# Kernel optimization log

Measured on AMD Instinct MI355X. Metric: run time of the kernel, lower is better.

## Reference

```python
import jax, jax.numpy as jnp
import numpy as np

B0, C0, H0, W0 = 2, 64, 48, 48
BR, DI, NS, RK, K = 128, 128, 16, 4, 4
EPS = 1e-5


def _bn_relu(x, g, b):
    # eval-mode BatchNorm2d (running mean 0, var 1) followed by ReLU; x is NCHW
    return jax.nn.relu(x * (g / jnp.sqrt(1.0 + EPS))[None, :, None, None] + b[None, :, None, None])


def _c1(x, w):
    # 1x1 conv, w: (O, C, 1, 1)
    return jnp.einsum('bchw,oc->bohw', x, w[:, :, 0, 0])


def _avgpool(x, k, s, p):
    # torch AvgPool2d with count_include_pad=True -> divide by k*k
    y = jax.lax.reduce_window(x, 0.0, jax.lax.add, (1, 1, k, k), (1, 1, s, s), ((0, 0), (0, 0), (p, p), (p, p)))
    return y / float(k * k)


def _resize(x, h, w):
    # bilinear, align_corners=False (half-pixel), NCHW
    return jax.image.resize(x, (x.shape[0], x.shape[1], h, w), 'bilinear')


def _pappm(x, s0_g, s0_b, s0_w, s1_g, s1_b, s1_w, s2_g, s2_b, s2_w, s3_g, s3_b, s3_w, s4_g, s4_b, s4_w, comp_g, comp_b, comp_w, sc_g, sc_b, sc_w):
    h, w = x.shape[2], x.shape[3]
    x0 = _c1(_bn_relu(x, s0_g, s0_b), s0_w)
    y1 = _c1(_bn_relu(_avgpool(x, 3, 1, 1), s1_g, s1_b), s1_w) + x0  # stride-1 pool keeps size
    y2 = _resize(_c1(_bn_relu(_avgpool(x, 5, 2, 2), s2_g, s2_b), s2_w), h, w) + x0
    y3 = _resize(_c1(_bn_relu(_avgpool(x, 9, 4, 4), s3_g, s3_b), s3_w), h, w) + x0
    y4 = _c1(_bn_relu(x.mean((2, 3), keepdims=True), s4_g, s4_b), s4_w) + x0  # 1x1 -> broadcast
    cat = jnp.concatenate([x0, y1, y2, y3, y4], axis=1)  # (B, 5*BR, H, W)
    comp = jax.lax.conv_general_dilated(_bn_relu(cat, comp_g, comp_b), comp_w, (1, 1), ((1, 1), (1, 1)), dimension_numbers=('NCHW', 'OIHW', 'NCHW'))
    return comp + _c1(_bn_relu(x, sc_g, sc_b), sc_w)


def _ss2d(xin, in_proj_w, dw_w, dw_b, x_proj_w, dt_w, dt_b, A_logs, Ds, ln_g, ln_b, out_proj_w):
    # xin: (B, H, W, d_model)
    Bb, Hh, Ww, _ = xin.shape
    xz = xin @ in_proj_w.T                      # (B,H,W,2*DI)
    xc, z = jnp.split(xz, 2, axis=-1)
    xc = jnp.transpose(xc, (0, 3, 1, 2))        # (B,DI,H,W)
    xc = jax.lax.conv_general_dilated(xc, dw_w, (1, 1), ((1, 1), (1, 1)), dimension_numbers=('NCHW', 'OIHW', 'NCHW'), feature_group_count=DI)
    xc = jax.nn.silu(xc + dw_b[None, :, None, None])
    L = Hh * Ww
    x_hw = xc.reshape(Bb, DI, L)
    x_wh = jnp.transpose(xc, (0, 1, 3, 2)).reshape(Bb, DI, L)
    xs = jnp.stack([x_hw, x_wh, x_hw[:, :, ::-1], x_wh[:, :, ::-1]], axis=1)  # (B,K,DI,L)
    x_dbl = jnp.einsum('bkdl,kcd->bkcl', xs, x_proj_w)
    dts, Bm, Cm = jnp.split(x_dbl, [RK, RK + NS], axis=2)  # (B,K,RK,L),(B,K,NS,L),(B,K,NS,L)
    delta = jax.nn.softplus(jnp.einsum('bkrl,kdr->bkdl', dts, dt_w) + dt_b[None, :, :, None])  # (B,K,DI,L)
    A = -jnp.exp(A_logs).reshape(K, DI, NS)
    a = jnp.exp(delta[..., None] * A[None, :, :, None, :])                    # (B,K,DI,L,NS)
    bu = (delta * xs)[..., None] * jnp.transpose(Bm, (0, 1, 3, 2))[:, :, None]  # (B,K,DI,L,NS)

    def comb(e1, e2):
        a1, b1 = e1
        a2, b2 = e2
        return a2 * a1, a2 * b1 + b2

    _, hst = jax.lax.associative_scan(comb, (a, bu), axis=3)  # h_t = a_t*h_{t-1} + b_t
    y = jnp.einsum('bkdln,bknl->bkdl', hst, Cm) + xs * Ds.reshape(K, DI)[None, :, :, None]
    inv = y[:, 2:4][:, :, :, ::-1]
    y3 = jnp.transpose(y[:, 1].reshape(Bb, DI, Ww, Hh), (0, 1, 3, 2)).reshape(Bb, DI, L)
    y4 = jnp.transpose(inv[:, 1].reshape(Bb, DI, Ww, Hh), (0, 1, 3, 2)).reshape(Bb, DI, L)
    ys = jnp.transpose(y[:, 0] + inv[:, 0] + y3 + y4, (0, 2, 1)).reshape(Bb, Hh, Ww, DI)
    mu = ys.mean(-1, keepdims=True)
    var = jnp.mean((ys - mu) ** 2, -1, keepdims=True)
    yn = (ys - mu) / jnp.sqrt(var + EPS) * ln_g + ln_b
    return (yn * jax.nn.silu(z)) @ out_proj_w.T  # (B,H,W,d_model)


def setup_inputs():
    key = jax.random.key(0)
    ks = iter(jax.random.split(key, 32))
    nrm = lambda shp, s: jax.random.normal(next(ks), shp, jnp.float32) * s
    d = {}
    d['x'] = nrm((B0, C0, H0, W0), 1.0)
    for nm in ['s0', 's1', 's2', 's3', 's4']:
        d[nm + '_g'] = jnp.ones((C0,), jnp.float32)
        d[nm + '_b'] = jnp.zeros((C0,), jnp.float32)
        d[nm + '_w'] = nrm((BR, C0, 1, 1), (2.0 / C0) ** 0.5)
    d['comp_g'] = jnp.ones((5 * BR,), jnp.float32)
    d['comp_b'] = jnp.zeros((5 * BR,), jnp.float32)
    d['comp_w'] = nrm((C0, 5 * BR, 3, 3), (2.0 / (5 * BR * 9)) ** 0.5)
    d['sc_g'] = jnp.ones((C0,), jnp.float32)
    d['sc_b'] = jnp.zeros((C0,), jnp.float32)
    d['sc_w'] = nrm((C0, C0, 1, 1), (2.0 / C0) ** 0.5)
    d['in_proj_w'] = nrm((2 * DI, C0), C0 ** -0.5)
    d['dw_w'] = nrm((DI, 1, 3, 3), 0.3)
    d['dw_b'] = jnp.zeros((DI,), jnp.float32)
    d['x_proj_w'] = nrm((K, RK + 2 * NS, DI), DI ** -0.5)
    d['dt_w'] = nrm((K, DI, RK), RK ** -0.5)
    d['dt_b'] = jnp.log(jnp.expm1(jnp.asarray(0.01, jnp.float32))) * jnp.ones((K, DI), jnp.float32)
    d['A_logs'] = jnp.tile(jnp.log(jnp.arange(1, NS + 1, dtype=jnp.float32))[None], (K * DI, 1))
    d['Ds'] = jnp.ones((K * DI,), jnp.float32)
    d['ln_g'] = jnp.ones((DI,), jnp.float32)
    d['ln_b'] = jnp.zeros((DI,), jnp.float32)
    d['out_proj_w'] = nrm((C0, DI), DI ** -0.5)
    d['fc1_w'] = nrm((BR, C0, 1, 1), C0 ** -0.5)
    d['fc1_b'] = jnp.zeros((BR,), jnp.float32)
    d['fc2_w'] = nrm((C0, BR, 1, 1), BR ** -0.5)
    d['fc2_b'] = jnp.zeros((C0,), jnp.float32)
    return d


def reference(x, s0_g, s0_b, s0_w, s1_g, s1_b, s1_w, s2_g, s2_b, s2_w, s3_g, s3_b, s3_w, s4_g, s4_b, s4_w, comp_g, comp_b, comp_w, sc_g, sc_b, sc_w, in_proj_w, dw_w, dw_b, x_proj_w, dt_w, dt_b, A_logs, Ds, ln_g, ln_b, out_proj_w, fc1_w, fc1_b, fc2_w, fc2_b):
    p = _pappm(x, s0_g, s0_b, s0_w, s1_g, s1_b, s1_w, s2_g, s2_b, s2_w, s3_g, s3_b, s3_w, s4_g, s4_b, s4_w, comp_g, comp_b, comp_w, sc_g, sc_b, sc_w)
    a = _ss2d(jnp.transpose(p, (0, 2, 3, 1)), in_proj_w, dw_w, dw_b, x_proj_w, dt_w, dt_b, A_logs, Ds, ln_g, ln_b, out_proj_w)
    x1 = jnp.transpose(a, (0, 3, 1, 2))  # (B,C0,H,W)
    h1 = jax.nn.silu(_c1(x1, fc1_w) + fc1_b[None, :, None, None])
    return _c1(h1, fc2_w) + fc2_b[None, :, None, None] + x1
```

## Files before the change

kernel.cpp:

```cpp
#include <hip/hip_runtime.h>
#include <math.h>

constexpr int cB = 2, cC = 64, cH = 48, cW = 48, cL = 48 * 48;
constexpr int cBR = 128, cDI = 128, cNS = 16, cRK = 4, cK = 4;
constexpr float cEPS = 1e-5f;
constexpr int NCH = 32;
constexpr int CHL = cL / NCH;
constexpr int KTOT = 5824;

typedef unsigned short u16;
typedef unsigned int u32;
typedef short s16x8 __attribute__((ext_vector_type(8)));
typedef float f32x4 __attribute__((ext_vector_type(4)));

__device__ __forceinline__ float bnrelu(float v, float g, float b) {
    float y = v * (g * rsqrtf(1.0f + cEPS)) + b;
    return y > 0.f ? y : 0.f;
}
__device__ __forceinline__ float silu(float v) {
    return v / (1.f + expf(-v));
}
__device__ __forceinline__ u16 f2bf(float f) {
    u32 u = __float_as_uint(f);
    u = (u + 0x7fffu + ((u >> 16) & 1u)) >> 16;
    return (u16)u;
}
__device__ __forceinline__ s16x8 cvt8(const float* p) {
    s16x8 r;
#pragma unroll
    for (int i = 0; i < 8; i++) r[i] = (short)f2bf(p[i]);
    return r;
}
__device__ __forceinline__ float row_sum16(float v) {
    v += __int_as_float(__builtin_amdgcn_update_dpp(0, __float_as_int(v), 0xB1, 0xF, 0xF, true));
    v += __int_as_float(__builtin_amdgcn_update_dpp(0, __float_as_int(v), 0x4E, 0xF, 0xF, true));
    v += __int_as_float(__builtin_amdgcn_update_dpp(0, __float_as_int(v), 0x124, 0xF, 0xF, true));
    v += __int_as_float(__builtin_amdgcn_update_dpp(0, __float_as_int(v), 0x128, 0xF, 0xF, true));
    return v;
}

__global__ void __launch_bounds__(256) k_pp(const float* __restrict__ x,
                                            float* __restrict__ pool5, float* __restrict__ pool9,
                                            float* __restrict__ gmean,
                                            const float* __restrict__ cw, const float* __restrict__ scw,
                                            const float* __restrict__ s0w, const float* __restrict__ s1w,
                                            const float* __restrict__ ipw, const float* __restrict__ xpw,
                                            const float* __restrict__ dww,
                                            const float* __restrict__ s2w, const float* __restrict__ s3w,
                                            u16* __restrict__ w8, u16* __restrict__ wcat,
                                            u16* __restrict__ ipk, u16* __restrict__ xpk,
                                            float* __restrict__ dwk, u16* __restrict__ c1k) {
    __shared__ float sm[4];
    int blk = blockIdx.x;
    int t = threadIdx.x;
    if (blk < 288) {
        int idx = blk * 256 + t;
        int w = idx % 24, h = (idx / 24) % 24, bc = idx / 576;
        const float* p = x + bc * cL;
        float s = 0.f;
        for (int kh = 0; kh < 5; kh++) {
            int hh = h * 2 - 2 + kh; if (hh < 0 || hh >= cH) continue;
            for (int kw = 0; kw < 5; kw++) {
                int ww = w * 2 - 2 + kw; if (ww < 0 || ww >= cW) continue;
                s += p[hh * cW + ww];
            }
        }
        pool5[idx] = s * (1.f / 25.f);
    } else if (blk < 360) {
        int idx = (blk - 288) * 256 + t;
        int w = idx % 12, h = (idx / 12) % 12, bc = idx / 144;
        const float* p = x + bc * cL;
        float s = 0.f;
        for (int kh = 0; kh < 9; kh++) {
            int hh = h * 4 - 4 + kh; if (hh < 0 || hh >= cH) continue;
            for (int kw = 0; kw < 9; kw++) {
                int ww = w * 4 - 4 + kw; if (ww < 0 || ww >= cW) continue;
                s += p[hh * cW + ww];
            }
        }
        pool9[idx] = s * (1.f / 81.f);
    } else if (blk < 488) {
        int bc = blk - 360;
        const float* p = x + bc * cL;
        float s = 0.f;
        for (int i = t; i < cL; i += 256) s += p[i];
        for (int m = 32; m > 0; m >>= 1) s += __shfl_down(s, m);
        if ((t & 63) == 0) sm[t >> 6] = s;
        __syncthreads();
        if (t == 0) gmean[bc] = (sm[0] + sm[1] + sm[2] + sm[3]) * (1.f / cL);
    } else if (blk < 1944) {
        int idx = (blk - 488) * 256 + t;
        int o = idx / KTOT, kx = idx % KTOT;
        float v;
        if (kx < 5760) { int tap = kx / 640, ch = kx % 640; v = cw[(o * 640 + ch) * 9 + tap]; }
        else v = scw[o * 64 + (kx - 5760)];
        w8[(((size_t)(kx >> 3) * 64) + o) * 8 + (kx & 7)] = f2bf(v);
    } else if (blk < 2008) {
        int idx = (blk - 1944) * 256 + t;
        int g = idx >> 13, r = idx & 8191;
        int o = r >> 6, c = r & 63;
        float v = (g ? s1w : s0w)[r];
        int kt = c >> 5, q = (c >> 3) & 3, j = c & 7, nt = o >> 4, ln = o & 15;
        wcat[(size_t)((((g * 2 + kt) * 4 + q) * 8 + nt) * 16 + ln) * 8 + j] = f2bf(v);
    } else if (blk < 2072) {
        int idx = (blk - 2008) * 256 + t;
        int o = idx >> 6, c = idx & 63;
        int kt = c >> 5, q = (c >> 3) & 3, j = c & 7, nt = o >> 4, ln = o & 15;
        ipk[(size_t)(((kt * 4 + q) * 16 + nt) * 16 + ln) * 8 + j] = f2bf(ipw[idx]);
    } else if (blk < 2144) {
        int idx = (blk - 2072) * 256 + t;
        int o = idx >> 7, d = idx & 127;
        int kt = d >> 5, q = (d >> 3) & 3, j = d & 7, nt = o >> 4, ln = o & 15;
        xpk[(size_t)(((kt * 4 + q) * 9 + nt) * 16 + ln) * 8 + j] = f2bf(xpw[idx]);
    } else if (blk < 2149) {
        int idx = (blk - 2144) * 256 + t;
        if (idx < 1152) {
            int tap = idx >> 7, ch = idx & 127;
            dwk[idx] = dww[ch * 9 + tap];
        }
    } else {
        int idx = (blk - 2149) * 256 + t;
        int g = idx >> 13, r = idx & 8191;
        int o = r >> 6, c = r & 63;
        float v = (g ? s3w : s2w)[r];
        int kt = c >> 5, q = (c >> 3) & 3, j = c & 7, nt = o >> 4, ln = o & 15;
        c1k[(size_t)((((g * 2 + kt) * 4 + q) * 8 + nt) * 16 + ln) * 8 + j] = f2bf(v);
    }
}

__global__ void __launch_bounds__(256) k_c1m(const float* __restrict__ pool5, const float* __restrict__ pool9,
                                             const float* __restrict__ gm,
                                             const float* __restrict__ s2g, const float* __restrict__ s2b,
                                             const float* __restrict__ s3g, const float* __restrict__ s3b,
                                             const float* __restrict__ s4g, const float* __restrict__ s4b,
                                             const float* __restrict__ s4w, const u16* __restrict__ c1k,
                                             float* __restrict__ c2cl, float* __restrict__ c3cl,
                                             float* __restrict__ c4) {
    int blk = blockIdx.x, t = threadIdx.x;
    if (blk >= 90) {
        int b = blk - 90;
        __shared__ float v[64];
        if (t < 64) v[t] = bnrelu(gm[b * 64 + t], s4g[t], s4b[t]);
        __syncthreads();
        if (t < 128) {
            const float* wr = s4w + t * 64;
            float acc = 0.f;
#pragma unroll 16
            for (int c = 0; c < 64; c++) acc += v[c] * wr[c];
            c4[b * 128 + t] = acc;
        }
        return;
    }
    int set, b, pp0, HW;
    const float *in, *g, *bb;
    float* outp;
    if (blk < 72) { set = 0; b = blk / 36; pp0 = (blk % 36) * 16; HW = 576; in = pool5; g = s2g; bb = s2b; outp = c2cl + (size_t)b * 576 * 128; }
    else { int r = blk - 72; set = 1; b = r / 9; pp0 = (r % 9) * 16; HW = 144; in = pool9; g = s3g; bb = s3b; outp = c3cl + (size_t)b * 144 * 128; }
    __shared__ u16 av16[16][72];
#pragma unroll
    for (int i = 0; i < 4; i++) {
        int id = i * 256 + t;
        int c = id >> 4, p = id & 15;
        av16[p][c] = f2bf(bnrelu(in[(size_t)(b * 64 + c) * HW + pp0 + p], g[c], bb[c]));
    }
    __syncthreads();
    int wv = t >> 6, lane = t & 63, ln = lane & 15, q = lane >> 4;
    f32x4 acc[2] = {};
#pragma unroll
    for (int kt = 0; kt < 2; kt++) {
        s16x8 a = *(const s16x8*)(&av16[ln][kt * 32 + q * 8]);
#pragma unroll
        for (int jn = 0; jn < 2; jn++) {
            int nt = wv * 2 + jn;
            s16x8 bfr = *(const s16x8*)(c1k + (size_t)((((set * 2 + kt) * 4 + q) * 8 + nt) * 16 + ln) * 8);
            acc[jn] = __builtin_amdgcn_mfma_f32_16x16x32_bf16(a, bfr, acc[jn], 0, 0, 0);
        }
    }
#pragma unroll
    for (int jn = 0; jn < 2; jn++) {
        int o = (wv * 2 + jn) * 16 + ln;
#pragma unroll
        for (int r = 0; r < 4; r++)
            outp[(size_t)(pp0 + q * 4 + r) * 128 + o] = acc[jn][r];
    }
}

__global__ void __launch_bounds__(512) k_cat2(
    const float* __restrict__ x, const float* __restrict__ c4,
    const float* __restrict__ s0g, const float* __restrict__ s0b,
    const float* __restrict__ s1g, const float* __restrict__ s1b,
    const float* __restrict__ scg, const float* __restrict__ scb,
    const float* __restrict__ cg, const float* __restrict__ cbb,
    const u16* __restrict__ wcat, const float* __restrict__ c2cl, const float* __restrict__ c3cl,
    u16* __restrict__ catbf, u16* __restrict__ xbf) {
    int blk = blockIdx.x;
    int b = blk / 144;
    int l0 = (blk % 144) * 16;
    int hrow = l0 / cW, w0g = l0 % cW;
    int t = threadIdx.x;
    __shared__ float xst[64][3][19];
    __shared__ float axv[16][68];
    __shared__ float ap3[16][68];
    __shared__ u16 axc[16][66];
#pragma unroll
    for (int i = 0; i < 7; i++) {
        int id = i * 512 + t;
        if (id < 3456) {
            int c = id / 54, rem = id % 54, rw = rem / 18, wi = rem % 18;
            int hh = hrow + rw - 1, ww = w0g + wi - 1;
            float v = 0.f;
            if (hh >= 0 && hh < cH && ww >= 0 && ww < cW)
                v = x[(size_t)(b * 64 + c) * cL + hh * cW + ww];
            xst[c][rw][wi] = v;
        }
    }
    __syncthreads();
#pragma unroll
    for (int i = 0; i < 2; i++) {
        int id = i * 512 + t;
        int c = id >> 4, p = id & 15;
        float xv = xst[c][1][p + 1];
        float s9 = 0.f;
#pragma unroll
        for (int rw = 0; rw < 3; rw++)
#pragma unroll
            for (int wi = 0; wi < 3; wi++)
                s9 += xst[c][rw][p + wi];
        axv[p][c] = bnrelu(xv, s0g[c], s0b[c]);
        ap3[p][c] = bnrelu(s9 * (1.f / 9.f), s1g[c], s1b[c]);
        axc[p][c] = f2bf(bnrelu(xv, scg[c], scb[c]));
    }
    __syncthreads();
#pragma unroll
    for (int i = 0; i < 2; i++) {
        int idx = i * 512 + t;
        int pp = idx >> 6, cc = idx & 63;
        xbf[((size_t)b * cL + l0 + pp) * 64 + cc] = axc[pp][cc];
    }
    int wv = t >> 6, lane = t & 63, ln = lane & 15, q = lane >> 4;
    f32x4 ax = {};
    f32x4 ay = {};
#pragma unroll
    for (int kt = 0; kt < 2; kt++) {
        s16x8 a0 = cvt8(&axv[ln][kt * 32 + q * 8]);
        s16x8 a1 = cvt8(&ap3[ln][kt * 32 + q * 8]);
        s16x8 b0 = *(const s16x8*)(wcat + (size_t)((((0 * 2 + kt) * 4 + q) * 8 + wv) * 16 + ln) * 8);
        s16x8 b1 = *(const s16x8*)(wcat + (size_t)((((1 * 2 + kt) * 4 + q) * 8 + wv) * 16 + ln) * 8);
        ax = __builtin_amdgcn_mfma_f32_16x16x32_bf16(a0, b0, ax, 0, 0, 0);
        ay = __builtin_amdgcn_mfma_f32_16x16x32_bf16(a1, b1, ay, 0, 0, 0);
    }
    float sy2 = hrow * 0.5f - 0.25f;
    float fy2 = floorf(sy2); int iy2 = (int)fy2; float ay2 = sy2 - fy2;
    int y20 = min(max(iy2, 0), 23), y21 = min(max(iy2 + 1, 0), 23);
    float sy3 = hrow * 0.25f - 0.375f;
    float fy3 = floorf(sy3); int iy3 = (int)fy3; float ay3 = sy3 - fy3;
    int y30 = min(max(iy3, 0), 11), y31 = min(max(iy3 + 1, 0), 11);
    const float* c2b = c2cl + (size_t)b * 576 * 128;
    const float* c3b = c3cl + (size_t)b * 144 * 128;
    int ch = wv * 16 + ln;
    float c4v = c4[b * 128 + ch];
#pragma unroll
    for (int r = 0; r < 4; r++) {
        int pp = q * 4 + r;
        int wq = w0g + pp;
        float sx2 = wq * 0.5f - 0.25f;
        float fx2 = floorf(sx2); int ix2 = (int)fx2; float ax2 = sx2 - fx2;
        int x20 = min(max(ix2, 0), 23), x21 = min(max(ix2 + 1, 0), 23);
        float sx3 = wq * 0.25f - 0.375f;
        float fx3 = floorf(sx3); int ix3 = (int)fx3; float ax3 = sx3 - fx3;
        int x30 = min(max(ix3, 0), 11), x31 = min(max(ix3 + 1, 0), 11);
        float v00 = c2b[(y20 * 24 + x20) * 128 + ch], v01 = c2b[(y20 * 24 + x21) * 128 + ch];
        float v10 = c2b[(y21 * 24 + x20) * 128 + ch], v11 = c2b[(y21 * 24 + x21) * 128 + ch];
        float t0 = v00 + (v01 - v00) * ax2, t1 = v10 + (v11 - v10) * ax2;
        float u2v = t0 + (t1 - t0) * ay2;
        float w00 = c3b[(y30 * 12 + x30) * 128 + ch], w01 = c3b[(y30 * 12 + x31) * 128 + ch];
        float w10 = c3b[(y31 * 12 + x30) * 128 + ch], w11 = c3b[(y31 * 12 + x31) * 128 + ch];
        float s0_ = w00 + (w01 - w00) * ax3, s1_ = w10 + (w11 - w10) * ax3;
        float u3v = s0_ + (s1_ - s0_) * ay3;
        float x0 = ax[r];
        float y1 = ay[r] + x0;
        float y2 = x0 + u2v;
        float y3 = x0 + u3v;
        float y4 = x0 + c4v;
        u16* base = catbf + ((size_t)b * cL + l0 + pp) * 640;
        base[ch]       = f2bf(bnrelu(x0, cg[ch],       cbb[ch]));
        base[128 + ch] = f2bf(bnrelu(y1, cg[128 + ch], cbb[128 + ch]));
        base[256 + ch] = f2bf(bnrelu(y2, cg[256 + ch], cbb[256 + ch]));
        base[384 + ch] = f2bf(bnrelu(y3, cg[384 + ch], cbb[384 + ch]));
        base[512 + ch] = f2bf(bnrelu(y4, cg[512 + ch], cbb[512 + ch]));
    }
}

__global__ void __launch_bounds__(512) k_compip(const u16* __restrict__ catbf,
                                                const u16* __restrict__ xbf,
                                                const u16* __restrict__ w8,
                                                const u16* __restrict__ ipk,
                                                float* __restrict__ xc, float* __restrict__ z) {
    int pix0 = blockIdx.x * 16;
    int b = pix0 / cL;
    int t = threadIdx.x;
    int wv = t >> 6, lane = t & 63, ln = lane & 15, q = lane >> 4;
    __shared__ float pl[8][16][68];
    __shared__ u16 pv16[16][72];
    int la = (pix0 + ln) - b * cL;
    int h = la / cW, w = la % cW;
    f32x4 acc[4] = {};
    int ks0 = wv * 23;
    int kcnt = (wv == 7) ? 21 : 23;
    for (int i = 0; i < kcnt; i++) {
        int ks = ks0 + i;
        s16x8 av;
        if (ks < 180) {
            int s = ks / 20;
            int cc = ks - s * 20;
            int s3 = s / 3;
            int kh = s3 - 1, kw = s - s3 * 3 - 1;
            int hh = h + kh, ww = w + kw;
            bool ok = (hh >= 0) && (hh < cH) && (ww >= 0) && (ww < cW);
            const u16* ap = catbf + (((size_t)b * cL + hh * cW + ww) * 640 + cc * 32 + q * 8);
            if (ok) av = *(const s16x8*)ap;
            else av = s16x8{0, 0, 0, 0, 0, 0, 0, 0};
        } else {
            int cc = ks - 180;
            av = *(const s16x8*)(xbf + (size_t)(pix0 + ln) * 64 + cc * 32 + q * 8);
        }
        const u16* wrow = w8 + ((size_t)ks * 4 + q) * 512;
#pragma unroll
        for (int j = 0; j < 4; j++) {
            s16x8 bv = *(const s16x8*)(wrow + (size_t)(j * 16 + ln) * 8);
            acc[j] = __builtin_amdgcn_mfma_f32_16x16x32_bf16(av, bv, acc[j], 0, 0, 0);
        }
    }
#pragma unroll
    for (int j = 0; j < 4; j++)
#pragma unroll
        for (int r = 0; r < 4; r++)
            pl[wv][q * 4 + r][j * 16 + ln] = acc[j][r];
    __syncthreads();
#pragma unroll
    for (int e = 0; e < 2; e++) {
        int id = e * 512 + t;
        int p = id >> 6, c = id & 63;
        float s = 0.f;
#pragma unroll
        for (int w2 = 0; w2 < 8; w2++) s += pl[w2][p][c];
        pv16[p][c] = f2bf(s);
    }
    __syncthreads();
    f32x4 a2[2] = {};
#pragma unroll
    for (int kt = 0; kt < 2; kt++) {
        s16x8 a = *(const s16x8*)(&pv16[ln][kt * 32 + q * 8]);
#pragma unroll
        for (int jn = 0; jn < 2; jn++) {
            int nt = wv * 2 + jn;
            s16x8 bfr = *(const s16x8*)(ipk + (size_t)(((kt * 4 + q) * 16 + nt) * 16 + ln) * 8);
            a2[jn] = __builtin_amdgcn_mfma_f32_16x16x32_bf16(a, bfr, a2[jn], 0, 0, 0);
        }
    }
#pragma unroll
    for (int jn = 0; jn < 2; jn++) {
        int o = (wv * 2 + jn) * 16 + ln;
#pragma unroll
        for (int r = 0; r < 4; r++) {
            int p = q * 4 + r;
            if (o < 128) xc[((size_t)pix0 + p) * 128 + o] = a2[jn][r];
            else         z[((size_t)pix0 + p) * 128 + (o - 128)] = a2[jn][r];
        }
    }
}

__global__ void __launch_bounds__(256) k_dw(const float* __restrict__ xc, const float* __restrict__ dwk,
                                            const float* __restrict__ dwb, float* __restrict__ xca) {
    int idx = blockIdx.x * 256 + threadIdx.x;
    int d4 = idx & 31;
    int rest = idx >> 5;
    int l = rest % cL, b = rest / cL;
    int h = l / cW, w = l % cW;
    const f32x4* xb = (const f32x4*)xc + (size_t)b * cL * 32;
    const f32x4* kb = (const f32x4*)dwk;
    f32x4 acc = ((const f32x4*)dwb)[d4];
#pragma unroll
    for (int i = 0; i < 3; i++) {
        int hh = h + i - 1; if (hh < 0 || hh >= cH) continue;
#pragma unroll
        for (int j = 0; j < 3; j++) {
            int ww = w + j - 1; if (ww < 0 || ww >= cW) continue;
            f32x4 v = xb[(size_t)(hh * cW + ww) * 32 + d4];
            f32x4 kv = kb[(i * 3 + j) * 32 + d4];
            acc += v * kv;
        }
    }
    f32x4 r;
#pragma unroll
    for (int c = 0; c < 4; c++) r[c] = silu(acc[c]);
    ((f32x4*)xca)[idx] = r;
}

__global__ void __launch_bounds__(1024) k_xdbl4(const float* __restrict__ xca, const u16* __restrict__ xpk,
                                                const float* __restrict__ dtw, const float* __restrict__ dtb,
                                                float* __restrict__ bc, float* __restrict__ delta) {
    int blk = blockIdx.x;
    int b = blk / 144;
    int l0 = (blk % 144) * 16;
    int t = threadIdx.x;
    __shared__ float av[16][132];
    __shared__ float Dt[16][148];
#pragma unroll
    for (int i = 0; i < 2; i++) {
        int id = i * 1024 + t;
        int d = id & 127, p = id >> 7;
        av[p][d] = xca[((size_t)b * cL + l0 + p) * 128 + d];
    }
    __syncthreads();
    int wv = t >> 6, lane = t & 63, ln = lane & 15, q = lane >> 4;
    if (wv < 9) {
        int nt = wv;
        f32x4 acc = {};
#pragma unroll
        for (int kt = 0; kt < 4; kt++) {
            s16x8 a = cvt8(&av[ln][kt * 32 + q * 8]);
            s16x8 bfr = *(const s16x8*)(xpk + (size_t)(((kt * 4 + q) * 9 + nt) * 16 + ln) * 8);
            acc = __builtin_amdgcn_mfma_f32_16x16x32_bf16(a, bfr, acc, 0, 0, 0);
        }
#pragma unroll
        for (int r = 0; r < 4; r++)
            Dt[q * 4 + r][nt * 16 + ln] = acc[r];
    }
    __syncthreads();
#pragma unroll
    for (int i = 0; i < 2; i++) {
        int id = i * 1024 + t;
        int cc = id & 31, kk = (id >> 5) & 3, p = id >> 7;
        bc[((size_t)(b * 4 + kk) * cL + l0 + p) * 32 + cc] = Dt[p][kk * 36 + 4 + cc];
    }
    {
        int d = t & 127;
        int kk = (t >> 7) & 3;
        int p0 = t >> 9;
        const float* wd = dtw + (size_t)(kk * 128 + d) * 4;
        float w0 = wd[0], w1 = wd[1], w2 = wd[2], w3 = wd[3];
        float bb = dtb[kk * 128 + d];
        float* dout = delta + ((size_t)(b * 4 + kk) * cL + l0) * 128 + d;
#pragma unroll
        for (int i = 0; i < 8; i++) {
            int p = p0 + i * 2;
            float pre = bb + w0 * Dt[p][kk * 36] + w1 * Dt[p][kk * 36 + 1]
                      + w2 * Dt[p][kk * 36 + 2] + w3 * Dt[p][kk * 36 + 3];
            float dl = pre > 20.f ? pre : log1pf(expf(pre));
            dout[(size_t)p * 128] = dl;
        }
    }
}

__device__ __forceinline__ int xs_index(int k, int l) {
    int lp = (k & 2) ? (cL - 1 - l) : l;
    if (k & 1) { int w = lp / cH, h = lp % cH; return h * cW + w; }
    return lp;
}

__global__ void __launch_bounds__(256) k_scan1(const float* __restrict__ delta, const float* __restrict__ xca,
                                               const float* __restrict__ bc, const float* __restrict__ Alogs,
                                               float* __restrict__ Pend, float* __restrict__ hend) {
    int blk = blockIdx.x;
    int c = blk & 31;
    if (c == NCH - 1) return;
    int g = blk >> 5;
    int dgq = g & 7, bk = g >> 3;
    int k = bk & 3, b = bk >> 2;
    int t = threadIdx.x;
    int n = t & 15;
    int d = dgq * 16 + (t >> 4);
    float A = -expf(Alogs[(k * 128 + d) * 16 + n]);
    const float* dp = delta + (size_t)bk * cL * 128 + d;
    const float* xp = xca + (size_t)b * cL * 128 + d;
    const float* bp = bc + (size_t)bk * cL * 32 + n;
    int off = xs_index(k, c * CHL);
    int step = (k == 0) ? 1 : (k == 1) ? cW : (k == 2) ? -1 : -cW;
    float P = 1.f, h = 0.f;
#pragma unroll 4
    for (int i = 0; i < CHL; i++) {
        float dl = dp[(size_t)off * 128];
        float a = expf(dl * A);
        h = a * h + dl * xp[(size_t)off * 128] * bp[(size_t)off * 32];
        P *= a;
        off += step;
        if (off >= cL) off -= (cL - 1);
        else if (off < 0) off += (cL - 1);
    }
    Pend[(size_t)blk * 256 + t] = P;
    hend[(size_t)blk * 256 + t] = h;
}

__global__ void __launch_bounds__(256) k_scan2(const float* __restrict__ Pend, float* __restrict__ hend) {
    int id = blockIdx.x * 256 + threadIdx.x;
    int t = id & 255;
    int g = id >> 8;
    float h = 0.f;
    for (int c = 0; c < NCH; c++) {
        size_t idx = ((size_t)g * NCH + c) * 256 + t;
        float tmp = hend[idx];
        float Pv = Pend[idx];
        hend[idx] = h;
        h = Pv * h + tmp;
    }
}

__global__ void __launch_bounds__(256) k_scan3(const float* __restrict__ delta, const float* __restrict__ xca,
                                               const float* __restrict__ bc, const float* __restrict__ Alogs,
                                               const float* __restrict__ Dsv, const float* __restrict__ hinb,
                                               float* __restrict__ y) {
    int blk = blockIdx.x;
    int c = blk & 31;
    int g = blk >> 5;
    int dgq = g & 7, bk = g >> 3;
    int k = bk & 3, b = bk >> 2;
    int t = threadIdx.x;
    int n = t & 15;
    int d = dgq * 16 + (t >> 4);
    float A = -expf(Alogs[(k * 128 + d) * 16 + n]);
    float Dsd = Dsv[k * 128 + d];
    const float* dp = delta + (size_t)bk * cL * 128 + d;
    const float* xp = xca + (size_t)b * cL * 128 + d;
    const float* bp = bc + (size_t)bk * cL * 32 + n;
    const float* cp = bc + (size_t)bk * cL * 32 + 16 + n;
    float* yb = y + (size_t)bk * cL * 128 + d;
    int off = xs_index(k, c * CHL);
    int step = (k == 0) ? 1 : (k == 1) ? cW : (k == 2) ? -1 : -cW;
    float h = hinb[(size_t)blk * 256 + t];
#pragma unroll 2
    for (int i = 0; i < CHL; i++) {
        float dl = dp[(size_t)off * 128];
        float xv = xp[(size_t)off * 128];
        float a = expf(dl * A);
        h = a * h + dl * xv * bp[(size_t)off * 32];
        float contrib = row_sum16(h * cp[(size_t)off * 32]);
        if (n == 0) yb[(size_t)off * 128] = contrib + xv * Dsd;
        off += step;
        if (off >= cL) off -= (cL - 1);
        else if (off < 0) off += (cL - 1);
    }
}

__global__ void __launch_bounds__(256) k_tail(const float* __restrict__ y, const float* __restrict__ z,
                                              const float* __restrict__ lng, const float* __restrict__ lnb,
                                              const float* __restrict__ opw,
                                              const float* __restrict__ f1w, const float* __restrict__ f1b,
                                              const float* __restrict__ f2w, const float* __restrict__ f2b,
                                              float* __restrict__ out) {
    int blk = blockIdx.x;
    int b = blk / 576;
    int l0 = (blk % 576) * 4;
    int t = threadIdx.x;
    __shared__ float v[4][132];
    __shared__ float x1s[4][68];
    __shared__ float h1s[4][132];
    __shared__ float mus[4], rss[4];
    const float* yb = y + (size_t)b * 4 * cL * 128;
#pragma unroll
    for (int i = 0; i < 2; i++) {
        int id = i * 256 + t;
        int d = id & 127, p = id >> 7;
        size_t base = (size_t)(l0 + p) * 128 + d;
        v[p][d] = yb[base] + yb[(size_t)cL * 128 + base] + yb[(size_t)2 * cL * 128 + base] + yb[(size_t)3 * cL * 128 + base];
    }
    __syncthreads();
    if (t < 64) {
        int p = t >> 4, c8 = (t & 15) * 8;
        float s = 0.f;
#pragma unroll
        for (int j = 0; j < 8; j++) s += v[p][c8 + j];
        s = row_sum16(s);
        float mu = s * (1.f / 128.f);
        float s2 = 0.f;
#pragma unroll
        for (int j = 0; j < 8; j++) { float dv = v[p][c8 + j] - mu; s2 += dv * dv; }
        s2 = row_sum16(s2);
        if ((t & 15) == 0) { mus[p] = mu; rss[p] = rsqrtf(s2 * (1.f / 128.f) + cEPS); }
    }
    __syncthreads();
#pragma unroll
    for (int i = 0; i < 2; i++) {
        int id = i * 256 + t;
        int d = id & 127, p = id >> 7;
        float zz = z[((size_t)b * cL + l0 + p) * 128 + d];
        v[p][d] = ((v[p][d] - mus[p]) * rss[p] * lng[d] + lnb[d]) * silu(zz);
    }
    __syncthreads();
    {
        int p = t & 3, o = t >> 2;
        const float* wr = opw + o * 128;
        float acc = 0.f;
#pragma unroll 16
        for (int d2 = 0; d2 < 128; d2++) acc += v[p][d2] * wr[d2];
        x1s[p][o] = acc;
    }
    __syncthreads();
#pragma unroll
    for (int i = 0; i < 2; i++) {
        int id = i * 256 + t;
        int p = id & 3, j = id >> 2;
        const float* wr = f1w + j * 64;
        float acc = f1b[j];
#pragma unroll 16
        for (int c = 0; c < 64; c++) acc += x1s[p][c] * wr[c];
        h1s[p][j] = silu(acc);
    }
    __syncthreads();
    {
        int p = t & 3, o = t >> 2;
        const float* wr = f2w + o * 128;
        float acc = f2b[o];
#pragma unroll 16
        for (int j = 0; j < 128; j++) acc += h1s[p][j] * wr[j];
        out[((size_t)b * 64 + o) * cL + l0 + p] = acc + x1s[p][o];
    }
}

extern "C" void kernel_launch(void* const* d_in, const int* in_sizes, int n_in,
                              void* d_out, int out_size, void* d_ws, size_t ws_size,
                              hipStream_t stream) {
    (void)in_sizes; (void)n_in; (void)out_size; (void)ws_size;
    const float* x    = (const float*)d_in[0];
    const float* s0g  = (const float*)d_in[1];
    const float* s0b  = (const float*)d_in[2];
    const float* s0w  = (const float*)d_in[3];
    const float* s1g  = (const float*)d_in[4];
    const float* s1b  = (const float*)d_in[5];
    const float* s1w  = (const float*)d_in[6];
    const float* s2g  = (const float*)d_in[7];
    const float* s2b  = (const float*)d_in[8];
    const float* s2w  = (const float*)d_in[9];
    const float* s3g  = (const float*)d_in[10];
    const float* s3b  = (const float*)d_in[11];
    const float* s3w  = (const float*)d_in[12];
    const float* s4g  = (const float*)d_in[13];
    const float* s4b  = (const float*)d_in[14];
    const float* s4w  = (const float*)d_in[15];
    const float* cg   = (const float*)d_in[16];
    const float* cbb  = (const float*)d_in[17];
    const float* cw   = (const float*)d_in[18];
    const float* scg  = (const float*)d_in[19];
    const float* scb  = (const float*)d_in[20];
    const float* scw  = (const float*)d_in[21];
    const float* ipw  = (const float*)d_in[22];
    const float* dww  = (const float*)d_in[23];
    const float* dwb  = (const float*)d_in[24];
    const float* xpw  = (const float*)d_in[25];
    const float* dtw  = (const float*)d_in[26];
    const float* dtb  = (const float*)d_in[27];
    const float* Alog = (const float*)d_in[28];
    const float* Dsv  = (const float*)d_in[29];
    const float* lng  = (const float*)d_in[30];
    const float* lnb  = (const float*)d_in[31];
    const float* opw  = (const float*)d_in[32];
    const float* f1w  = (const float*)d_in[33];
    const float* f1b  = (const float*)d_in[34];
    const float* f2w  = (const float*)d_in[35];
    const float* f2b  = (const float*)d_in[36];
    float* out = (float*)d_out;

    float* ws = (float*)d_ws;
    size_t off = 0;
    float* pool5  = ws + off; off += 73728;
    float* pool9  = ws + off; off += 18432;
    float* gmean  = ws + off; off += 128;
    float* c2cl   = ws + off; off += 147456;
    float* c3cl   = ws + off; off += 36864;
    float* c4     = ws + off; off += 256;
    u16*   catbf  = (u16*)(ws + off); off += 1474560;
    u16*   xbf    = (u16*)(ws + off); off += 147456;
    u16*   w8     = (u16*)(ws + off); off += 186368;
    u16*   wcat   = (u16*)(ws + off); off += 8192;
    u16*   ipk    = (u16*)(ws + off); off += 8192;
    u16*   c1k    = (u16*)(ws + off); off += 8192;
    if (off < 2359296) off = 2359296;
    float* xc     = ws + off; off += 589824;
    u16*   xpk    = (u16*)(ws + off); off += 9216;
    float* dwk    = ws + off; off += 1280;
    float* xca    = ws + off; off += 589824;
    float* zbuf   = ws + off; off += 589824;
    float* bcbuf  = ws + off; off += 589824;
    float* Pend   = ws + off; off += 524288;
    float* ybuf   = ws + off; off += 2359296;
    off += 294912;
    float* delta  = ws + 0;
    float* hend   = xc;

    k_pp<<<2213, 256, 0, stream>>>(x, pool5, pool9, gmean,
                                   cw, scw, s0w, s1w, ipw, xpw, dww, s2w, s3w,
                                   w8, wcat, ipk, xpk, dwk, c1k);
    k_c1m<<<92, 256, 0, stream>>>(pool5, pool9, gmean, s2g, s2b, s3g, s3b, s4g, s4b, s4w,
                                  c1k, c2cl, c3cl, c4);
    k_cat2<<<cB * 144, 512, 0, stream>>>(x, c4, s0g, s0b, s1g, s1b, scg, scb, cg, cbb,
                                         wcat, c2cl, c3cl, catbf, xbf);
    k_compip<<<cB * cL / 16, 512, 0, stream>>>(catbf, xbf, w8, ipk, xc, zbuf);
    k_dw<<<cB * cL * 128 / 4 / 256, 256, 0, stream>>>(xc, dwk, dwb, xca);
    k_xdbl4<<<cB * 144, 1024, 0, stream>>>(xca, xpk, dtw, dtb, bcbuf, delta);
    k_scan1<<<64 * NCH, 256, 0, stream>>>(delta, xca, bcbuf, Alog, Pend, hend);
    k_scan2<<<64, 256, 0, stream>>>(Pend, hend);
    k_scan3<<<64 * NCH, 256, 0, stream>>>(delta, xca, bcbuf, Alog, Dsv, hend, ybuf);
    k_tail<<<cB * 576, 256, 0, stream>>>(ybuf, zbuf, lng, lnb, opw, f1w, f1b, f2w, f2b, out);
}
```

Before: 290.6 us.

## Fuse depthwise conv into x-projection kernel and fold chunk-carry scan into scan3

The depthwise 3x3 conv plus SiLU moves into k_xdbl4. Each block stages a 3x18x128 halo of xc in shared memory and computes the activations for its 16 pixels directly, writing xca out for the scan kernels. The separate k_scan2 kernel is removed: each k_scan3 block serially combines the Pend/hend chunk carries of all preceding chunks to get its starting state. This saves two kernel launches and a global round trip for xca. In exchange, the serial prefix is recomputed redundantly in every scan3 block and the halo staging loads extra rows.

```diff
diff --git a/kernel.cpp b/kernel.cpp
--- a/kernel.cpp
+++ b/kernel.cpp
@@ -370,47 +370,48 @@
     }
 }
 
-__global__ void __launch_bounds__(256) k_dw(const float* __restrict__ xc, const float* __restrict__ dwk,
-                                            const float* __restrict__ dwb, float* __restrict__ xca) {
-    int idx = blockIdx.x * 256 + threadIdx.x;
-    int d4 = idx & 31;
-    int rest = idx >> 5;
-    int l = rest % cL, b = rest / cL;
-    int h = l / cW, w = l % cW;
-    const f32x4* xb = (const f32x4*)xc + (size_t)b * cL * 32;
-    const f32x4* kb = (const f32x4*)dwk;
-    f32x4 acc = ((const f32x4*)dwb)[d4];
-#pragma unroll
-    for (int i = 0; i < 3; i++) {
-        int hh = h + i - 1; if (hh < 0 || hh >= cH) continue;
-#pragma unroll
-        for (int j = 0; j < 3; j++) {
-            int ww = w + j - 1; if (ww < 0 || ww >= cW) continue;
-            f32x4 v = xb[(size_t)(hh * cW + ww) * 32 + d4];
-            f32x4 kv = kb[(i * 3 + j) * 32 + d4];
-            acc += v * kv;
-        }
-    }
-    f32x4 r;
-#pragma unroll
-    for (int c = 0; c < 4; c++) r[c] = silu(acc[c]);
-    ((f32x4*)xca)[idx] = r;
-}
-
-__global__ void __launch_bounds__(1024) k_xdbl4(const float* __restrict__ xca, const u16* __restrict__ xpk,
+__global__ void __launch_bounds__(1024) k_xdbl4(const float* __restrict__ xc, const float* __restrict__ dwk,
+                                                const float* __restrict__ dwb,
+                                                const u16* __restrict__ xpk,
                                                 const float* __restrict__ dtw, const float* __restrict__ dtb,
-                                                float* __restrict__ bc, float* __restrict__ delta) {
+                                                float* __restrict__ bc, float* __restrict__ delta,
+                                                float* __restrict__ xca) {
     int blk = blockIdx.x;
     int b = blk / 144;
     int l0 = (blk % 144) * 16;
+    int hrow = l0 / cW, w0 = l0 % cW;
     int t = threadIdx.x;
+    __shared__ float hal[3][18][128];
     __shared__ float av[16][132];
     __shared__ float Dt[16][148];
+#pragma unroll
+    for (int i = 0; i < 7; i++) {
+        int id = i * 1024 + t;
+        if (id < 6912) {
+            int d = id & 127;
+            int rem = id >> 7;
+            int wi = rem % 18, rw = rem / 18;
+            int hh = hrow + rw - 1, ww = w0 + wi - 1;
+            float v = 0.f;
+            if (hh >= 0 && hh < cH && ww >= 0 && ww < cW)
+                v = xc[((size_t)b * cL + hh * cW + ww) * 128 + d];
+            hal[rw][wi][d] = v;
+        }
+    }
+    __syncthreads();
 #pragma unroll
     for (int i = 0; i < 2; i++) {
         int id = i * 1024 + t;
         int d = id & 127, p = id >> 7;
-        av[p][d] = xca[((size_t)b * cL + l0 + p) * 128 + d];
+        float acc = dwb[d];
+#pragma unroll
+        for (int rw = 0; rw < 3; rw++)
+#pragma unroll
+            for (int wi = 0; wi < 3; wi++)
+                acc += hal[rw][p + wi][d] * dwk[(rw * 3 + wi) * 128 + d];
+        float v = silu(acc);
+        av[p][d] = v;
+        xca[((size_t)b * cL + l0 + p) * 128 + d] = v;
     }
     __syncthreads();
     int wv = t >> 6, lane = t & 63, ln = lane & 15, q = lane >> 4;
@@ -439,13 +440,13 @@
         int kk = (t >> 7) & 3;
         int p0 = t >> 9;
         const float* wd = dtw + (size_t)(kk * 128 + d) * 4;
-        float w0 = wd[0], w1 = wd[1], w2 = wd[2], w3 = wd[3];
+        float w0_ = wd[0], w1 = wd[1], w2 = wd[2], w3 = wd[3];
         float bb = dtb[kk * 128 + d];
         float* dout = delta + ((size_t)(b * 4 + kk) * cL + l0) * 128 + d;
 #pragma unroll
         for (int i = 0; i < 8; i++) {
             int p = p0 + i * 2;
-            float pre = bb + w0 * Dt[p][kk * 36] + w1 * Dt[p][kk * 36 + 1]
+            float pre = bb + w0_ * Dt[p][kk * 36] + w1 * Dt[p][kk * 36 + 1]
                       + w2 * Dt[p][kk * 36 + 2] + w3 * Dt[p][kk * 36 + 3];
             float dl = pre > 20.f ? pre : log1pf(expf(pre));
             dout[(size_t)p * 128] = dl;
@@ -492,23 +493,10 @@
     hend[(size_t)blk * 256 + t] = h;
 }
 
-__global__ void __launch_bounds__(256) k_scan2(const float* __restrict__ Pend, float* __restrict__ hend) {
-    int id = blockIdx.x * 256 + threadIdx.x;
-    int t = id & 255;
-    int g = id >> 8;
-    float h = 0.f;
-    for (int c = 0; c < NCH; c++) {
-        size_t idx = ((size_t)g * NCH + c) * 256 + t;
-        float tmp = hend[idx];
-        float Pv = Pend[idx];
-        hend[idx] = h;
-        h = Pv * h + tmp;
-    }
-}
-
 __global__ void __launch_bounds__(256) k_scan3(const float* __restrict__ delta, const float* __restrict__ xca,
                                                const float* __restrict__ bc, const float* __restrict__ Alogs,
-                                               const float* __restrict__ Dsv, const float* __restrict__ hinb,
+                                               const float* __restrict__ Dsv,
+                                               const float* __restrict__ Pend, const float* __restrict__ hend,
                                                float* __restrict__ y) {
     int blk = blockIdx.x;
     int c = blk & 31;
@@ -518,6 +506,11 @@
     int t = threadIdx.x;
     int n = t & 15;
     int d = dgq * 16 + (t >> 4);
+    float h = 0.f;
+    for (int cc = 0; cc < c; cc++) {
+        size_t idx = ((size_t)g * NCH + cc) * 256 + t;
+        h = Pend[idx] * h + hend[idx];
+    }
     float A = -expf(Alogs[(k * 128 + d) * 16 + n]);
     float Dsd = Dsv[k * 128 + d];
     const float* dp = delta + (size_t)bk * cL * 128 + d;
@@ -527,7 +520,6 @@
     float* yb = y + (size_t)bk * cL * 128 + d;
     int off = xs_index(k, c * CHL);
     int step = (k == 0) ? 1 : (k == 1) ? cW : (k == 2) ? -1 : -cW;
-    float h = hinb[(size_t)blk * 256 + t];
 #pragma unroll 2
     for (int i = 0; i < CHL; i++) {
         float dl = dp[(size_t)off * 128];
@@ -695,10 +687,8 @@
     k_cat2<<<cB * 144, 512, 0, stream>>>(x, c4, s0g, s0b, s1g, s1b, scg, scb, cg, cbb,
                                          wcat, c2cl, c3cl, catbf, xbf);
     k_compip<<<cB * cL / 16, 512, 0, stream>>>(catbf, xbf, w8, ipk, xc, zbuf);
-    k_dw<<<cB * cL * 128 / 4 / 256, 256, 0, stream>>>(xc, dwk, dwb, xca);
-    k_xdbl4<<<cB * 144, 1024, 0, stream>>>(xca, xpk, dtw, dtb, bcbuf, delta);
+    k_xdbl4<<<cB * 144, 1024, 0, stream>>>(xc, dwk, dwb, xpk, dtw, dtb, bcbuf, delta, xca);
     k_scan1<<<64 * NCH, 256, 0, stream>>>(delta, xca, bcbuf, Alog, Pend, hend);
-    k_scan2<<<64, 256, 0, stream>>>(Pend, hend);
-    k_scan3<<<64 * NCH, 256, 0, stream>>>(delta, xca, bcbuf, Alog, Dsv, hend, ybuf);
+    k_scan3<<<64 * NCH, 256, 0, stream>>>(delta, xca, bcbuf, Alog, Dsv, Pend, hend, ybuf);
     k_tail<<<cB * 576, 256, 0, stream>>>(ybuf, zbuf, lng, lnb, opw, f1w, f1b, f2w, f2b, out);
 }
```

Measured after the change: 286.4 us. About the same (-1.5%).
